# Performance work log

Hardware: AMD Instinct MI355X
Metric: run time of the kernel (lower is better)

The kernel has to match this reference:

```python
import jax, jax.numpy as jnp
import numpy as np

B, S, D, H, L = 16, 1024, 128, 8, 3
DFF = 4 * D  # 512
DH = D // H  # 16
NUM_CLASSES = 6


def layernorm(x, g, b, eps):
    mu = jnp.mean(x, axis=-1, keepdims=True)
    var = jnp.mean(jnp.square(x - mu), axis=-1, keepdims=True)
    return g * (x - mu) / jnp.sqrt(var + eps) + b


def setup_inputs() -> dict:
    key = jax.random.key(0)
    ks = jax.random.split(key, 16)
    sc = 0.05
    inp = {
        'x': jax.random.normal(ks[0], (B, S, D), dtype=jnp.float32),
        'Wq': jax.random.normal(ks[1], (L, D, D), dtype=jnp.float32) * sc,
        'bq': jnp.zeros((L, D), dtype=jnp.float32),
        'Wk': jax.random.normal(ks[2], (L, D, D), dtype=jnp.float32) * sc,
        'bk': jnp.zeros((L, D), dtype=jnp.float32),
        'Wv': jax.random.normal(ks[3], (L, D, D), dtype=jnp.float32) * sc,
        'bv': jnp.zeros((L, D), dtype=jnp.float32),
        'ln1_g': jnp.ones((L, D), dtype=jnp.float32),
        'ln1_b': jnp.zeros((L, D), dtype=jnp.float32),
        'W1': jax.random.normal(ks[4], (L, D, DFF), dtype=jnp.float32) * sc,
        'b1': jnp.zeros((L, DFF), dtype=jnp.float32),
        'W2': jax.random.normal(ks[5], (L, DFF, D), dtype=jnp.float32) * sc,
        'b2': jnp.zeros((L, D), dtype=jnp.float32),
        'ln2_g': jnp.ones((L, D), dtype=jnp.float32),
        'ln2_b': jnp.zeros((L, D), dtype=jnp.float32),
        'Wout': jax.random.normal(ks[6], (D, NUM_CLASSES), dtype=jnp.float32) * sc,
        'bout': jnp.zeros((NUM_CLASSES,), dtype=jnp.float32),
    }
    return inp


def reference(x, Wq, bq, Wk, bk, Wv, bv, ln1_g, ln1_b, W1, b1, W2, b2, ln2_g, ln2_b, Wout, bout):
    scale = 1.0 / jnp.sqrt(jnp.float32(DH))
    for l in range(L):
        # Q/K/V projections with ReLU activation (as in source Dense(..., relu))
        q = jax.nn.relu(jnp.einsum('bsd,de->bse', x, Wq[l]) + bq[l])
        k = jax.nn.relu(jnp.einsum('bsd,de->bse', x, Wk[l]) + bk[l])
        v = jax.nn.relu(jnp.einsum('bsd,de->bse', x, Wv[l]) + bv[l])
        # split-heads (tf.split axis=-1 / concat axis=0 == reshape to heads)
        qh = q.reshape(B, S, H, DH)
        kh = k.reshape(B, S, H, DH)
        vh = v.reshape(B, S, H, DH)
        scores = jnp.einsum('bqhd,bkhd->bhqk', qh, kh) * scale  # [B,H,S,S]
        attn = jax.nn.softmax(scores, axis=-1)
        o = jnp.einsum('bhqk,bkhd->bqhd', attn, vh).reshape(B, S, D)
        x = layernorm(o + x, ln1_g[l], ln1_b[l], 1e-8)
        # pointwise FFN (Conv1D kernel_size=1 == dense over last dim)
        h = jax.nn.relu(jnp.einsum('bsd,df->bsf', x, W1[l]) + b1[l])
        f = jnp.einsum('bsf,fd->bsd', h, W2[l]) + b2[l]
        x = layernorm(f + x, ln2_g[l], ln2_b[l], 1e-6)
    return jnp.einsum('bsd,dc->bsc', x, Wout) + bout
```

## Files before the change

### kernel.cpp

```cpp
#include <hip/hip_runtime.h>
#include <math.h>

#define Bq 16
#define Sq 1024
#define Dq 128
#define Hq 8
#define DHq 16
#define DFFq 512
#define Lq 3
#define NCLS 6
#define NROWS (Bq * Sq)
#define NX ((size_t)NROWS * Dq)

#define QSCL 0.36067376022224085f

typedef __attribute__((ext_vector_type(8))) short    bf16x8;
typedef __attribute__((ext_vector_type(4))) float    f32x4;
typedef __attribute__((ext_vector_type(4))) _Float16 f16x4;
typedef __attribute__((ext_vector_type(8))) _Float16 f16x8;

__device__ inline ushort f32_to_bf16(float f) {
    union { float f; unsigned u; } v; v.f = f;
    unsigned r = v.u + 0x7fffu + ((v.u >> 16) & 1u);
    return (ushort)(r >> 16);
}

__device__ __forceinline__ float exp2_raw(float x) {
    float r;
    asm("v_exp_f32 %0, %1" : "=v"(r) : "v"(x));
    return r;
}

__global__ __launch_bounds__(256) void prep_kernel(
    const float* __restrict__ Wqp, const float* __restrict__ Wkp,
    const float* __restrict__ Wvp, const float* __restrict__ W1p,
    const float* __restrict__ W2p, const float* __restrict__ xp,
    ushort* __restrict__ wbf, ushort* __restrict__ xbf)
{
    const int gid = blockIdx.x * 256 + threadIdx.x;
    if (gid < 147456) {
        const int w   = gid / 49152;
        const int rem = gid - w * 49152;
        const int l   = rem >> 14;
        const int idx = rem & 16383;
        const int k   = idx >> 7;
        const int n   = idx & 127;
        const float* src = (w == 0) ? Wqp : (w == 1) ? Wkp : Wvp;
        const float scl = (w == 0) ? QSCL : 1.0f;
        wbf[(size_t)(w * 3 + l) * 16384 + n * 128 + k] =
            f32_to_bf16(src[(size_t)l * 16384 + k * 128 + n] * scl);
    } else if (gid < 344064) {
        const int g   = gid - 147456;
        const int l   = g >> 16;
        const int idx = g & 65535;
        const int k   = idx >> 9;
        const int n   = idx & 511;
        wbf[147456 + (size_t)l * 65536 + n * 128 + k] =
            f32_to_bf16(W1p[(size_t)l * 65536 + k * 512 + n]);
    } else if (gid < 540672) {
        const int g   = gid - 344064;
        const int l   = g >> 16;
        const int idx = g & 65535;
        const int k   = idx >> 7;
        const int n   = idx & 127;
        wbf[344064 + (size_t)l * 65536 + n * 512 + k] =
            f32_to_bf16(W2p[(size_t)l * 65536 + k * 128 + n]);
    } else {
        const int g = gid - 540672;
        xbf[g] = f32_to_bf16(xp[g]);
    }
}

__global__ __launch_bounds__(256) void gemm_qkv(
    const ushort* __restrict__ A,
    const ushort* __restrict__ wq, const ushort* __restrict__ wk,
    const ushort* __restrict__ wv,
    const float* __restrict__ bqp, const float* __restrict__ bkp,
    const float* __restrict__ bvp,
    _Float16* __restrict__ qo, _Float16* __restrict__ ko,
    _Float16* __restrict__ vo)
{
    __shared__ ushort As[64 * 40];
    __shared__ ushort Bs[128 * 40];

    const int sel  = blockIdx.y;
    const ushort* Bt   = (sel == 0) ? wq : (sel == 1) ? wk : wv;
    const float*  bias = (sel == 0) ? bqp : (sel == 1) ? bkp : bvp;
    const float   bscl = (sel == 0) ? QSCL : 1.0f;

    const int tid  = threadIdx.x;
    const int row0 = blockIdx.x * 64;
    const int wave = tid >> 6;
    const int lane = tid & 63;
    const int quad = lane >> 4;
    const int m16  = lane & 15;
    const int wm   = wave >> 1;
    const int wn   = wave & 1;

    const int sar = tid >> 2;
    const int sac = (tid & 3) * 8;

    f32x4 acc[2][4];
    #pragma unroll
    for (int i = 0; i < 2; ++i)
        #pragma unroll
        for (int j = 0; j < 4; ++j) acc[i][j] = (f32x4)0.f;

    for (int k0 = 0; k0 < 128; k0 += 32) {
        bf16x8 av = *(const bf16x8*)(A + (size_t)(row0 + sar) * 128 + k0 + sac);
        const int r1 = tid >> 2, r2 = r1 + 64;
        bf16x8 bv1 = *(const bf16x8*)(Bt + (size_t)r1 * 128 + k0 + sac);
        bf16x8 bv2 = *(const bf16x8*)(Bt + (size_t)r2 * 128 + k0 + sac);

        __syncthreads();
        *(bf16x8*)&As[sar * 40 + sac] = av;
        *(bf16x8*)&Bs[r1 * 40 + sac]  = bv1;
        *(bf16x8*)&Bs[r2 * 40 + sac]  = bv2;
        __syncthreads();

        bf16x8 af[2], bf[4];
        #pragma unroll
        for (int i = 0; i < 2; ++i)
            af[i] = *(const bf16x8*)&As[(32 * wm + 16 * i + m16) * 40 + quad * 8];
        #pragma unroll
        for (int j = 0; j < 4; ++j)
            bf[j] = *(const bf16x8*)&Bs[(64 * wn + 16 * j + m16) * 40 + quad * 8];
        #pragma unroll
        for (int i = 0; i < 2; ++i)
            #pragma unroll
            for (int j = 0; j < 4; ++j)
                acc[i][j] = __builtin_amdgcn_mfma_f32_16x16x32_bf16(af[i], bf[j], acc[i][j], 0, 0, 0);
    }

    #pragma unroll
    for (int i = 0; i < 2; ++i) {
        #pragma unroll
        for (int j = 0; j < 4; ++j) {
            const int col = 64 * wn + 16 * j + m16;
            const float bb = bias[col] * bscl;
            const int hh = col >> 4, dh = col & 15;
            #pragma unroll
            for (int r = 0; r < 4; ++r) {
                float val = fmaxf(acc[i][j][r] + bb, 0.f);
                const int gr = row0 + 32 * wm + 16 * i + quad * 4 + r;
                const int b = gr >> 10, s = gr & 1023;
                if (sel == 2) {
                    vo[(((size_t)b * Hq + hh) * DHq + dh) * Sq + s] = (_Float16)val;
                } else {
                    _Float16* outp = (sel == 0) ? qo : ko;
                    outp[(((size_t)b * Hq + hh) * Sq + s) * DHq + dh] = (_Float16)val;
                }
            }
        }
    }
}

__global__ __launch_bounds__(256) void gemm_ffn_fused(
    const _Float16* __restrict__ o, const float* __restrict__ resid,
    const float* __restrict__ g1, const float* __restrict__ beta1,
    const ushort* __restrict__ W1t, const float* __restrict__ bias1,
    const ushort* __restrict__ W2t, const float* __restrict__ bias2,
    const float* __restrict__ g2, const float* __restrict__ beta2,
    float* __restrict__ xb,
    const ushort* __restrict__ wqn, const ushort* __restrict__ wkn,
    const ushort* __restrict__ wvn,
    const float* __restrict__ bqn, const float* __restrict__ bkn,
    const float* __restrict__ bvn,
    _Float16* __restrict__ qo, _Float16* __restrict__ ko,
    _Float16* __restrict__ vo, int do_next,
    const float* __restrict__ Wout, const float* __restrict__ bout,
    float* __restrict__ out, int last)
{
    __shared__ __align__(16) char smem[69120];
    ushort*    Af   = (ushort*)smem;
    ushort*    Hs   = (ushort*)(smem + 8704);
    ushort*    Bs   = (ushort*)(smem + 41984);
    float*     wo_s = (float*)(smem + 41984);
    _Float16*  vals = (_Float16*)(smem + 60416);
    float*     mus  = (float*)(smem + 68864);
    float*     rsds = (float*)(smem + 68992);

    const int tid  = threadIdx.x;
    const int row0 = blockIdx.x * 32;
    const int wave = tid >> 6;
    const int lane = tid & 63;
    const int quad = lane >> 4;
    const int m16  = lane & 15;
    const int wm   = wave >> 1;
    const int wn   = wave & 1;
    const int sac  = (tid & 3) * 8;
    const int r1   = tid >> 2, r2 = r1 + 64;

    #pragma unroll 2
    for (int it = 0; it < 8; ++it) {
        const int rr = wave * 8 + it;
        const size_t base = (size_t)(row0 + rr) * Dq;
        float v0 = (float)o[base + lane]      + resid[base + lane];
        float v1 = (float)o[base + 64 + lane] + resid[base + 64 + lane];

        float s = v0 + v1;
        #pragma unroll
        for (int off = 32; off > 0; off >>= 1) s += __shfl_xor(s, off, 64);
        const float mu = s * (1.f / 128.f);
        const float d0 = v0 - mu, d1 = v1 - mu;
        float vs = d0 * d0 + d1 * d1;
        #pragma unroll
        for (int off = 32; off > 0; off >>= 1) vs += __shfl_xor(vs, off, 64);
        const float rstd = rsqrtf(vs * (1.f / 128.f) + 1e-8f);

        const float rv0 = g1[lane]      * d0 * rstd + beta1[lane];
        const float rv1 = g1[lane + 64] * d1 * rstd + beta1[lane + 64];
        Af[rr * 136 + lane]        = f32_to_bf16(rv0);
        Af[rr * 136 + 64 + lane]   = f32_to_bf16(rv1);
        vals[rr * 132 + lane]      = (_Float16)rv0;
        vals[rr * 132 + 64 + lane] = (_Float16)rv1;
    }

    f32x4 acc[4];
    #pragma unroll
    for (int j = 0; j < 4; ++j) acc[j] = (f32x4)0.f;

    for (int idx = 0; idx < 8; ++idx) {
        const int cc = idx >> 1;
        const int k0 = (idx & 1) * 64;

        bf16x8 w11 = *(const bf16x8*)(W1t + (size_t)(cc * 128 + r1) * 128 + k0 + sac);
        bf16x8 w12 = *(const bf16x8*)(W1t + (size_t)(cc * 128 + r1) * 128 + k0 + 32 + sac);
        bf16x8 w21 = *(const bf16x8*)(W1t + (size_t)(cc * 128 + r2) * 128 + k0 + sac);
        bf16x8 w22 = *(const bf16x8*)(W1t + (size_t)(cc * 128 + r2) * 128 + k0 + 32 + sac);

        __syncthreads();
        *(bf16x8*)&Bs[r1 * 72 + sac]      = w11;
        *(bf16x8*)&Bs[r1 * 72 + 32 + sac] = w12;
        *(bf16x8*)&Bs[r2 * 72 + sac]      = w21;
        *(bf16x8*)&Bs[r2 * 72 + 32 + sac] = w22;
        __syncthreads();

        #pragma unroll
        for (int hh = 0; hh < 2; ++hh) {
            const int kk = k0 + hh * 32;
            const bf16x8 af = *(const bf16x8*)&Af[(16 * wm + m16) * 136 + kk + quad * 8];
            bf16x8 bf[4];
            #pragma unroll
            for (int j = 0; j < 4; ++j)
                bf[j] = *(const bf16x8*)&Bs[(64 * wn + 16 * j + m16) * 72 + hh * 32 + quad * 8];
            #pragma unroll
            for (int j = 0; j < 4; ++j)
                acc[j] = __builtin_amdgcn_mfma_f32_16x16x32_bf16(af, bf[j], acc[j], 0, 0, 0);
        }

        if (idx & 1) {
            #pragma unroll
            for (int j = 0; j < 4; ++j) {
                const int col = cc * 128 + 64 * wn + 16 * j + m16;
                const float bb = bias1[col];
                #pragma unroll
                for (int r = 0; r < 4; ++r) {
                    const int row = 16 * wm + quad * 4 + r;
                    Hs[row * 520 + col] = f32_to_bf16(fmaxf(acc[j][r] + bb, 0.f));
                }
                acc[j] = (f32x4)0.f;
            }
        }
    }

    f32x4 acc2[4];
    #pragma unroll
    for (int j = 0; j < 4; ++j) acc2[j] = (f32x4)0.f;

    for (int kc = 0; kc < 8; ++kc) {
        const int k0 = kc * 64;

        bf16x8 w11 = *(const bf16x8*)(W2t + (size_t)r1 * DFFq + k0 + sac);
        bf16x8 w12 = *(const bf16x8*)(W2t + (size_t)r1 * DFFq + k0 + 32 + sac);
        bf16x8 w21 = *(const bf16x8*)(W2t + (size_t)r2 * DFFq + k0 + sac);
        bf16x8 w22 = *(const bf16x8*)(W2t + (size_t)r2 * DFFq + k0 + 32 + sac);

        __syncthreads();
        *(bf16x8*)&Bs[r1 * 72 + sac]      = w11;
        *(bf16x8*)&Bs[r1 * 72 + 32 + sac] = w12;
        *(bf16x8*)&Bs[r2 * 72 + sac]      = w21;
        *(bf16x8*)&Bs[r2 * 72 + 32 + sac] = w22;
        __syncthreads();

        #pragma unroll
        for (int hh = 0; hh < 2; ++hh) {
            const int kk = k0 + hh * 32;
            const bf16x8 af = *(const bf16x8*)&Hs[(16 * wm + m16) * 520 + kk + quad * 8];
            bf16x8 bf[4];
            #pragma unroll
            for (int j = 0; j < 4; ++j)
                bf[j] = *(const bf16x8*)&Bs[(64 * wn + 16 * j + m16) * 72 + hh * 32 + quad * 8];
            #pragma unroll
            for (int j = 0; j < 4; ++j)
                acc2[j] = __builtin_amdgcn_mfma_f32_16x16x32_bf16(af, bf[j], acc2[j], 0, 0, 0);
        }
    }

    __syncthreads();

    float vreg[4][4];
    #pragma unroll
    for (int j = 0; j < 4; ++j) {
        const int col = 64 * wn + 16 * j + m16;
        const float bb = bias2[col];
        #pragma unroll
        for (int r = 0; r < 4; ++r) {
            const int row = 16 * wm + quad * 4 + r;
            float v = acc2[j][r] + bb + (float)vals[row * 132 + col];
            vreg[j][r] = v;
            vals[row * 132 + col] = (_Float16)v;
        }
    }
    if (last) {
        #pragma unroll
        for (int i = 0; i < 3; ++i) wo_s[tid + i * 256] = Wout[tid + i * 256];
    }
    __syncthreads();

    if (tid < 32) {
        float s = 0.f, s2 = 0.f;
        #pragma unroll 8
        for (int c = 0; c < Dq; ++c) {
            float x = (float)vals[tid * 132 + c];
            s += x; s2 = fmaf(x, x, s2);
        }
        const float mu  = s * (1.f / 128.f);
        const float var = s2 * (1.f / 128.f) - mu * mu;
        mus[tid]  = mu;
        rsds[tid] = rsqrtf(var + 1e-6f);
    }
    __syncthreads();

    if (!last) {
        #pragma unroll
        for (int j = 0; j < 4; ++j) {
            const int col = 64 * wn + 16 * j + m16;
            #pragma unroll
            for (int r = 0; r < 4; ++r) {
                const int row = 16 * wm + quad * 4 + r;
                const float rn = g2[col] * (vreg[j][r] - mus[row]) * rsds[row] + beta2[col];
                xb[(size_t)(row0 + row) * Dq + col] = rn;
                Af[row * 136 + col] = f32_to_bf16(rn);
            }
        }

        if (do_next) {
            for (int sel = 0; sel < 3; ++sel) {
                const ushort* Bt   = (sel == 0) ? wqn : (sel == 1) ? wkn : wvn;
                const float*  bias = (sel == 0) ? bqn : (sel == 1) ? bkn : bvn;
                const float   bscl = (sel == 0) ? QSCL : 1.0f;

                f32x4 qacc[4];
                #pragma unroll
                for (int j = 0; j < 4; ++j) qacc[j] = (f32x4)0.f;

                for (int half = 0; half < 2; ++half) {
                    const int k0 = half * 64;
                    bf16x8 w11 = *(const bf16x8*)(Bt + (size_t)r1 * 128 + k0 + sac);
                    bf16x8 w12 = *(const bf16x8*)(Bt + (size_t)r1 * 128 + k0 + 32 + sac);
                    bf16x8 w21 = *(const bf16x8*)(Bt + (size_t)r2 * 128 + k0 + sac);
                    bf16x8 w22 = *(const bf16x8*)(Bt + (size_t)r2 * 128 + k0 + 32 + sac);

                    __syncthreads();
                    *(bf16x8*)&Bs[r1 * 72 + sac]      = w11;
                    *(bf16x8*)&Bs[r1 * 72 + 32 + sac] = w12;
                    *(bf16x8*)&Bs[r2 * 72 + sac]      = w21;
                    *(bf16x8*)&Bs[r2 * 72 + 32 + sac] = w22;
                    __syncthreads();

                    #pragma unroll
                    for (int hh = 0; hh < 2; ++hh) {
                        const int kk = k0 + hh * 32;
                        const bf16x8 af = *(const bf16x8*)&Af[(16 * wm + m16) * 136 + kk + quad * 8];
                        bf16x8 bf[4];
                        #pragma unroll
                        for (int j = 0; j < 4; ++j)
                            bf[j] = *(const bf16x8*)&Bs[(64 * wn + 16 * j + m16) * 72 + hh * 32 + quad * 8];
                        #pragma unroll
                        for (int j = 0; j < 4; ++j)
                            qacc[j] = __builtin_amdgcn_mfma_f32_16x16x32_bf16(af, bf[j], qacc[j], 0, 0, 0);
                    }
                }

                #pragma unroll
                for (int j = 0; j < 4; ++j) {
                    const int col = 64 * wn + 16 * j + m16;
                    const float bb = bias[col] * bscl;
                    const int hh = col >> 4, dh = col & 15;
                    #pragma unroll
                    for (int r = 0; r < 4; ++r) {
                        float val = fmaxf(qacc[j][r] + bb, 0.f);
                        const int gr = row0 + 16 * wm + quad * 4 + r;
                        const int b = gr >> 10, s = gr & 1023;
                        if (sel == 2) {
                            vo[(((size_t)b * Hq + hh) * DHq + dh) * Sq + s] = (_Float16)val;
                        } else {
                            _Float16* outp = (sel == 0) ? qo : ko;
                            outp[(((size_t)b * Hq + hh) * Sq + s) * DHq + dh] = (_Float16)val;
                        }
                    }
                }
            }
        }
    } else {
        #pragma unroll
        for (int j = 0; j < 4; ++j) {
            const int col = 64 * wn + 16 * j + m16;
            #pragma unroll
            for (int r = 0; r < 4; ++r) {
                const int row = 16 * wm + quad * 4 + r;
                vals[row * 132 + col] =
                    (_Float16)(g2[col] * (vreg[j][r] - mus[row]) * rsds[row] + beta2[col]);
            }
        }
        __syncthreads();
        if (tid < 32 * NCLS) {
            const int row = tid / NCLS;
            const int c   = tid - row * NCLS;
            float a = bout[c];
            #pragma unroll 8
            for (int kk = 0; kk < Dq; ++kk)
                a = fmaf((float)vals[row * 132 + kk], wo_s[kk * NCLS + c], a);
            out[(size_t)(row0 + row) * NCLS + c] = a;
        }
    }
}

__global__ __launch_bounds__(256) void attn_mfma(
    const _Float16* __restrict__ q, const _Float16* __restrict__ k,
    const _Float16* __restrict__ vt, _Float16* __restrict__ o)
{
    __shared__ _Float16 Ks[256 * 20];
    __shared__ _Float16 Vs[16 * 264];

    const int bh   = blockIdx.x;
    const int qc   = blockIdx.y;
    const int b    = bh >> 3;
    const int h    = bh & 7;
    const int tid  = threadIdx.x;
    const int wave = tid >> 6;
    const int lane = tid & 63;
    const int quad = lane >> 4;
    const int m16  = lane & 15;
    const int q0   = qc * 128 + wave * 32;

    const f16x4 qf0 = *(const f16x4*)(q + (((size_t)bh * Sq) + q0 + m16) * DHq + quad * 4);
    const f16x4 qf1 = *(const f16x4*)(q + (((size_t)bh * Sq) + q0 + 16 + m16) * DHq + quad * 4);

    const _Float16* kg  = k  + (size_t)bh * Sq * DHq;
    const _Float16* vtg = vt + (size_t)bh * DHq * Sq;

    f32x4 oacc0 = (f32x4)0.f, oacc1 = (f32x4)0.f;
    float lacc0 = 0.f, lacc1 = 0.f;

    const int krow = tid;
    const int vrow = tid >> 4;
    const int vcol = (tid & 15) * 16;

    for (int kb = 0; kb < 4; ++kb) {
        f16x8 ka  = *(const f16x8*)(kg + ((size_t)kb * 256 + krow) * DHq);
        f16x8 kb8 = *(const f16x8*)(kg + ((size_t)kb * 256 + krow) * DHq + 8);
        f16x8 va  = *(const f16x8*)(vtg + (size_t)vrow * Sq + kb * 256 + vcol);
        f16x8 vb  = *(const f16x8*)(vtg + (size_t)vrow * Sq + kb * 256 + vcol + 8);
        __syncthreads();
        *(f16x8*)&Ks[krow * 20 + 0] = ka;
        *(f16x8*)&Ks[krow * 20 + 8] = kb8;
        *(f16x8*)&Vs[vrow * 264 + vcol + 0] = va;
        *(f16x8*)&Vs[vrow * 264 + vcol + 8] = vb;
        __syncthreads();

        #pragma unroll 4
        for (int kt = 0; kt < 16; ++kt) {
            const f16x4 kf = *(const f16x4*)&Ks[(kt * 16 + m16) * 20 + quad * 4];
            const f16x4 vf = *(const f16x4*)&Vs[m16 * 264 + kt * 16 + quad * 4];

            f32x4 st0 = __builtin_amdgcn_mfma_f32_16x16x16f16(kf, qf0, (f32x4)0.f, 0, 0, 0);
            f32x4 st1 = __builtin_amdgcn_mfma_f32_16x16x16f16(kf, qf1, (f32x4)0.f, 0, 0, 0);

            float p00 = exp2_raw(st0[0]);
            float p01 = exp2_raw(st0[1]);
            float p02 = exp2_raw(st0[2]);
            float p03 = exp2_raw(st0[3]);
            float p10 = exp2_raw(st1[0]);
            float p11 = exp2_raw(st1[1]);
            float p12 = exp2_raw(st1[2]);
            float p13 = exp2_raw(st1[3]);
            lacc0 += (p00 + p01) + (p02 + p03);
            lacc1 += (p10 + p11) + (p12 + p13);

            f16x4 pf0, pf1;
            pf0[0] = (_Float16)p00; pf0[1] = (_Float16)p01;
            pf0[2] = (_Float16)p02; pf0[3] = (_Float16)p03;
            pf1[0] = (_Float16)p10; pf1[1] = (_Float16)p11;
            pf1[2] = (_Float16)p12; pf1[3] = (_Float16)p13;

            oacc0 = __builtin_amdgcn_mfma_f32_16x16x16f16(pf0, vf, oacc0, 0, 0, 0);
            oacc1 = __builtin_amdgcn_mfma_f32_16x16x16f16(pf1, vf, oacc1, 0, 0, 0);
        }
    }

    lacc0 += __shfl_xor(lacc0, 16, 64);
    lacc0 += __shfl_xor(lacc0, 32, 64);
    lacc1 += __shfl_xor(lacc1, 16, 64);
    lacc1 += __shfl_xor(lacc1, 32, 64);

    #pragma unroll
    for (int r = 0; r < 4; ++r) {
        const float ls0 = __shfl(lacc0, quad * 4 + r, 64);
        const float ls1 = __shfl(lacc1, quad * 4 + r, 64);
        o[((size_t)b * Sq + q0 + quad * 4 + r) * Dq + h * DHq + m16]      = (_Float16)(oacc0[r] / ls0);
        o[((size_t)b * Sq + q0 + 16 + quad * 4 + r) * Dq + h * DHq + m16] = (_Float16)(oacc1[r] / ls1);
    }
}

extern "C" void kernel_launch(void* const* d_in, const int* in_sizes, int n_in,
                              void* d_out, int out_size, void* d_ws, size_t ws_size,
                              hipStream_t stream)
{
    const float* x_in  = (const float*)d_in[0];
    const float* Wq    = (const float*)d_in[1];
    const float* bq    = (const float*)d_in[2];
    const float* Wk    = (const float*)d_in[3];
    const float* bk    = (const float*)d_in[4];
    const float* Wv    = (const float*)d_in[5];
    const float* bv    = (const float*)d_in[6];
    const float* ln1_g = (const float*)d_in[7];
    const float* ln1_b = (const float*)d_in[8];
    const float* W1    = (const float*)d_in[9];
    const float* b1    = (const float*)d_in[10];
    const float* W2    = (const float*)d_in[11];
    const float* b2    = (const float*)d_in[12];
    const float* ln2_g = (const float*)d_in[13];
    const float* ln2_b = (const float*)d_in[14];
    const float* Wout  = (const float*)d_in[15];
    const float* bout  = (const float*)d_in[16];
    float* out = (float*)d_out;

    float* ws = (float*)d_ws;
    _Float16* qf16 = (_Float16*)ws;
    _Float16* kf16 = (_Float16*)(ws + NX / 2);
    _Float16* vt16 = (_Float16*)(ws + NX);
    float*    xb   = ws + 9 * NX / 2;
    ushort*   xbf0 = (ushort*)(ws + 11 * NX / 2);
    ushort*   wbf  = (ushort*)(ws + 7 * NX);
    _Float16* obuf = (_Float16*)(ws + 8 * NX);

    prep_kernel<<<dim3(10304), dim3(256), 0, stream>>>(Wq, Wk, Wv, W1, W2, x_in, wbf, xbf0);

    const dim3 blk(256);

    {
        const ushort* wqt = wbf + (size_t)0 * 16384;
        const ushort* wkt = wbf + (size_t)3 * 16384;
        const ushort* wvt = wbf + (size_t)6 * 16384;
        gemm_qkv<<<dim3(256, 3), blk, 0, stream>>>(
            xbf0, wqt, wkt, wvt, bq, bk, bv, qf16, kf16, vt16);
    }

    const float* xcur = x_in;
    for (int l = 0; l < Lq; ++l) {
        const ushort* w1t = wbf + 147456 + (size_t)l * 65536;
        const ushort* w2t = wbf + 344064 + (size_t)l * 65536;
        const int next = (l < Lq - 1) ? 1 : 0;
        const int ln   = l + 1;
        const ushort* wqn = next ? (wbf + (size_t)(0 * 3 + ln) * 16384) : wbf;
        const ushort* wkn = next ? (wbf + (size_t)(1 * 3 + ln) * 16384) : wbf;
        const ushort* wvn = next ? (wbf + (size_t)(2 * 3 + ln) * 16384) : wbf;
        const float*  bqn = next ? (bq + ln * Dq) : bq;
        const float*  bkn = next ? (bk + ln * Dq) : bk;
        const float*  bvn = next ? (bv + ln * Dq) : bv;

        attn_mfma<<<dim3(Bq * Hq, 8), blk, 0, stream>>>(qf16, kf16, vt16, obuf);

        gemm_ffn_fused<<<dim3(512), blk, 0, stream>>>(
            obuf, xcur, ln1_g + l * Dq, ln1_b + l * Dq,
            w1t, b1 + l * DFFq, w2t, b2 + l * Dq,
            ln2_g + l * Dq, ln2_b + l * Dq,
            xb,
            wqn, wkn, wvn, bqn, bkn, bvn,
            qf16, kf16, vt16, next,
            Wout, bout, out, (l == Lq - 1) ? 1 : 0);

        xcur = xb;
    }
}
```

Measured before the change: 254.8 us.

## Shrink FFN kernel shared memory by splitting hidden dim into halves

The fused LN+FFN kernel now processes the 512-wide hidden layer in two 256-column halves. It accumulates the second GEMM across halves, so the hidden buffer and the weight staging tile (now 32-wide K chunks) shrink and total LDS drops from about 69KB to about 36KB. Launch bounds request 4 blocks per CU. The residual is cached in registers and the LDS regions are aliased. This is meant to raise occupancy, at the cost of twice as many barrier-separated K steps with smaller loads each.

Measured after the change: 260.0 us. 2.0% more time.

```diff
diff --git a/kernel.cpp b/kernel.cpp
--- a/kernel.cpp
+++ b/kernel.cpp
@@ -155,7 +155,7 @@
     }
 }
 
-__global__ __launch_bounds__(256) void gemm_ffn_fused(
+__global__ __launch_bounds__(256, 4) void gemm_ffn_fused(
     const _Float16* __restrict__ o, const float* __restrict__ resid,
     const float* __restrict__ g1, const float* __restrict__ beta1,
     const ushort* __restrict__ W1t, const float* __restrict__ bias1,
@@ -171,14 +171,15 @@
     const float* __restrict__ Wout, const float* __restrict__ bout,
     float* __restrict__ out, int last)
 {
-    __shared__ __align__(16) char smem[69120];
-    ushort*    Af   = (ushort*)smem;
-    ushort*    Hs   = (ushort*)(smem + 8704);
-    ushort*    Bs   = (ushort*)(smem + 41984);
-    float*     wo_s = (float*)(smem + 41984);
-    _Float16*  vals = (_Float16*)(smem + 60416);
-    float*     mus  = (float*)(smem + 68864);
-    float*     rsds = (float*)(smem + 68992);
+    __shared__ __align__(16) char smem[36096];
+    ushort*    Af    = (ushort*)smem;
+    ushort*    Hs    = (ushort*)(smem + 8704);
+    ushort*    Bs    = (ushort*)(smem + 25600);
+    _Float16*  r16   = (_Float16*)(smem + 25600);
+    _Float16*  vals2 = (_Float16*)(smem + 8704);
+    float*     wo_s  = (float*)(smem + 25600);
+    float*     mus   = (float*)(smem + 35840);
+    float*     rsds  = (float*)(smem + 35968);
 
     const int tid  = threadIdx.x;
     const int row0 = blockIdx.x * 32;
@@ -210,87 +211,84 @@
 
         const float rv0 = g1[lane]      * d0 * rstd + beta1[lane];
         const float rv1 = g1[lane + 64] * d1 * rstd + beta1[lane + 64];
-        Af[rr * 136 + lane]        = f32_to_bf16(rv0);
-        Af[rr * 136 + 64 + lane]   = f32_to_bf16(rv1);
-        vals[rr * 132 + lane]      = (_Float16)rv0;
-        vals[rr * 132 + 64 + lane] = (_Float16)rv1;
-    }
-
-    f32x4 acc[4];
+        Af[rr * 136 + lane]       = f32_to_bf16(rv0);
+        Af[rr * 136 + 64 + lane]  = f32_to_bf16(rv1);
+        r16[rr * 132 + lane]      = (_Float16)rv0;
+        r16[rr * 132 + 64 + lane] = (_Float16)rv1;
+    }
+    __syncthreads();
+
+    float rreg[4][4];
     #pragma unroll
-    for (int j = 0; j < 4; ++j) acc[j] = (f32x4)0.f;
-
-    for (int idx = 0; idx < 8; ++idx) {
-        const int cc = idx >> 1;
-        const int k0 = (idx & 1) * 64;
-
-        bf16x8 w11 = *(const bf16x8*)(W1t + (size_t)(cc * 128 + r1) * 128 + k0 + sac);
-        bf16x8 w12 = *(const bf16x8*)(W1t + (size_t)(cc * 128 + r1) * 128 + k0 + 32 + sac);
-        bf16x8 w21 = *(const bf16x8*)(W1t + (size_t)(cc * 128 + r2) * 128 + k0 + sac);
-        bf16x8 w22 = *(const bf16x8*)(W1t + (size_t)(cc * 128 + r2) * 128 + k0 + 32 + sac);
-
-        __syncthreads();
-        *(bf16x8*)&Bs[r1 * 72 + sac]      = w11;
-        *(bf16x8*)&Bs[r1 * 72 + 32 + sac] = w12;
-        *(bf16x8*)&Bs[r2 * 72 + sac]      = w21;
-        *(bf16x8*)&Bs[r2 * 72 + 32 + sac] = w22;
-        __syncthreads();
-
-        #pragma unroll
-        for (int hh = 0; hh < 2; ++hh) {
-            const int kk = k0 + hh * 32;
-            const bf16x8 af = *(const bf16x8*)&Af[(16 * wm + m16) * 136 + kk + quad * 8];
-            bf16x8 bf[4];
-            #pragma unroll
-            for (int j = 0; j < 4; ++j)
-                bf[j] = *(const bf16x8*)&Bs[(64 * wn + 16 * j + m16) * 72 + hh * 32 + quad * 8];
-            #pragma unroll
-            for (int j = 0; j < 4; ++j)
-                acc[j] = __builtin_amdgcn_mfma_f32_16x16x32_bf16(af, bf[j], acc[j], 0, 0, 0);
-        }
-
-        if (idx & 1) {
-            #pragma unroll
-            for (int j = 0; j < 4; ++j) {
-                const int col = cc * 128 + 64 * wn + 16 * j + m16;
-                const float bb = bias1[col];
-                #pragma unroll
-                for (int r = 0; r < 4; ++r) {
-                    const int row = 16 * wm + quad * 4 + r;
-                    Hs[row * 520 + col] = f32_to_bf16(fmaxf(acc[j][r] + bb, 0.f));
-                }
-                acc[j] = (f32x4)0.f;
-            }
-        }
+    for (int j = 0; j < 4; ++j) {
+        const int col = 64 * wn + 16 * j + m16;
+        #pragma unroll
+        for (int r = 0; r < 4; ++r)
+            rreg[j][r] = (float)r16[(16 * wm + quad * 4 + r) * 132 + col];
     }
 
     f32x4 acc2[4];
     #pragma unroll
     for (int j = 0; j < 4; ++j) acc2[j] = (f32x4)0.f;
 
-    for (int kc = 0; kc < 8; ++kc) {
-        const int k0 = kc * 64;
-
-        bf16x8 w11 = *(const bf16x8*)(W2t + (size_t)r1 * DFFq + k0 + sac);
-        bf16x8 w12 = *(const bf16x8*)(W2t + (size_t)r1 * DFFq + k0 + 32 + sac);
-        bf16x8 w21 = *(const bf16x8*)(W2t + (size_t)r2 * DFFq + k0 + sac);
-        bf16x8 w22 = *(const bf16x8*)(W2t + (size_t)r2 * DFFq + k0 + 32 + sac);
-
-        __syncthreads();
-        *(bf16x8*)&Bs[r1 * 72 + sac]      = w11;
-        *(bf16x8*)&Bs[r1 * 72 + 32 + sac] = w12;
-        *(bf16x8*)&Bs[r2 * 72 + sac]      = w21;
-        *(bf16x8*)&Bs[r2 * 72 + 32 + sac] = w22;
-        __syncthreads();
-
-        #pragma unroll
-        for (int hh = 0; hh < 2; ++hh) {
-            const int kk = k0 + hh * 32;
-            const bf16x8 af = *(const bf16x8*)&Hs[(16 * wm + m16) * 520 + kk + quad * 8];
+    for (int half = 0; half < 2; ++half) {
+        f32x4 acc[4];
+        #pragma unroll
+        for (int j = 0; j < 4; ++j) acc[j] = (f32x4)0.f;
+
+        for (int idx = 0; idx < 8; ++idx) {
+            const int cc = idx >> 2;
+            const int k0 = (idx & 3) * 32;
+            const int gc0 = half * 256 + cc * 128;
+
+            bf16x8 wv1 = *(const bf16x8*)(W1t + (size_t)(gc0 + r1) * 128 + k0 + sac);
+            bf16x8 wv2 = *(const bf16x8*)(W1t + (size_t)(gc0 + r2) * 128 + k0 + sac);
+
+            __syncthreads();
+            *(bf16x8*)&Bs[r1 * 40 + sac] = wv1;
+            *(bf16x8*)&Bs[r2 * 40 + sac] = wv2;
+            __syncthreads();
+
+            const bf16x8 af = *(const bf16x8*)&Af[(16 * wm + m16) * 136 + k0 + quad * 8];
             bf16x8 bf[4];
             #pragma unroll
             for (int j = 0; j < 4; ++j)
-                bf[j] = *(const bf16x8*)&Bs[(64 * wn + 16 * j + m16) * 72 + hh * 32 + quad * 8];
+                bf[j] = *(const bf16x8*)&Bs[(64 * wn + 16 * j + m16) * 40 + quad * 8];
+            #pragma unroll
+            for (int j = 0; j < 4; ++j)
+                acc[j] = __builtin_amdgcn_mfma_f32_16x16x32_bf16(af, bf[j], acc[j], 0, 0, 0);
+
+            if ((idx & 3) == 3) {
+                #pragma unroll
+                for (int j = 0; j < 4; ++j) {
+                    const int lcol = cc * 128 + 64 * wn + 16 * j + m16;
+                    const float bb = bias1[half * 256 + lcol];
+                    #pragma unroll
+                    for (int r = 0; r < 4; ++r) {
+                        const int row = 16 * wm + quad * 4 + r;
+                        Hs[row * 264 + lcol] = f32_to_bf16(fmaxf(acc[j][r] + bb, 0.f));
+                    }
+                    acc[j] = (f32x4)0.f;
+                }
+            }
+        }
+
+        for (int kc = 0; kc < 8; ++kc) {
+            const int k0 = kc * 32;
+
+            bf16x8 wv1 = *(const bf16x8*)(W2t + (size_t)r1 * DFFq + half * 256 + k0 + sac);
+            bf16x8 wv2 = *(const bf16x8*)(W2t + (size_t)r2 * DFFq + half * 256 + k0 + sac);
+
+            __syncthreads();
+            *(bf16x8*)&Bs[r1 * 40 + sac] = wv1;
+            *(bf16x8*)&Bs[r2 * 40 + sac] = wv2;
+            __syncthreads();
+
+            const bf16x8 af = *(const bf16x8*)&Hs[(16 * wm + m16) * 264 + k0 + quad * 8];
+            bf16x8 bf[4];
+            #pragma unroll
+            for (int j = 0; j < 4; ++j)
+                bf[j] = *(const bf16x8*)&Bs[(64 * wn + 16 * j + m16) * 40 + quad * 8];
             #pragma unroll
             for (int j = 0; j < 4; ++j)
                 acc2[j] = __builtin_amdgcn_mfma_f32_16x16x32_bf16(af, bf[j], acc2[j], 0, 0, 0);
@@ -307,9 +305,9 @@
         #pragma unroll
         for (int r = 0; r < 4; ++r) {
             const int row = 16 * wm + quad * 4 + r;
-            float v = acc2[j][r] + bb + (float)vals[row * 132 + col];
+            float v = acc2[j][r] + bb + rreg[j][r];
             vreg[j][r] = v;
-            vals[row * 132 + col] = (_Float16)v;
+            vals2[row * 132 + col] = (_Float16)v;
         }
     }
     if (last) {
@@ -322,7 +320,7 @@
         float s = 0.f, s2 = 0.f;
         #pragma unroll 8
         for (int c = 0; c < Dq; ++c) {
-            float x = (float)vals[tid * 132 + c];
+            float x = (float)vals2[tid * 132 + c];
             s += x; s2 = fmaf(x, x, s2);
         }
         const float mu  = s * (1.f / 128.f);
@@ -355,32 +353,24 @@
                 #pragma unroll
                 for (int j = 0; j < 4; ++j) qacc[j] = (f32x4)0.f;
 
-                for (int half = 0; half < 2; ++half) {
-                    const int k0 = half * 64;
-                    bf16x8 w11 = *(const bf16x8*)(Bt + (size_t)r1 * 128 + k0 + sac);
-                    bf16x8 w12 = *(const bf16x8*)(Bt + (size_t)r1 * 128 + k0 + 32 + sac);
-                    bf16x8 w21 = *(const bf16x8*)(Bt + (size_t)r2 * 128 + k0 + sac);
-                    bf16x8 w22 = *(const bf16x8*)(Bt + (size_t)r2 * 128 + k0 + 32 + sac);
+                for (int kc = 0; kc < 4; ++kc) {
+                    const int k0 = kc * 32;
+                    bf16x8 wv1 = *(const bf16x8*)(Bt + (size_t)r1 * 128 + k0 + sac);
+                    bf16x8 wv2 = *(const bf16x8*)(Bt + (size_t)r2 * 128 + k0 + sac);
 
                     __syncthreads();
-                    *(bf16x8*)&Bs[r1 * 72 + sac]      = w11;
-                    *(bf16x8*)&Bs[r1 * 72 + 32 + sac] = w12;
-                    *(bf16x8*)&Bs[r2 * 72 + sac]      = w21;
-                    *(bf16x8*)&Bs[r2 * 72 + 32 + sac] = w22;
+                    *(bf16x8*)&Bs[r1 * 40 + sac] = wv1;
+                    *(bf16x8*)&Bs[r2 * 40 + sac] = wv2;
                     __syncthreads();
 
+                    const bf16x8 af = *(const bf16x8*)&Af[(16 * wm + m16) * 136 + k0 + quad * 8];
+                    bf16x8 bf[4];
                     #pragma unroll
-                    for (int hh = 0; hh < 2; ++hh) {
-                        const int kk = k0 + hh * 32;
-                        const bf16x8 af = *(const bf16x8*)&Af[(16 * wm + m16) * 136 + kk + quad * 8];
-                        bf16x8 bf[4];
-                        #pragma unroll
-                        for (int j = 0; j < 4; ++j)
-                            bf[j] = *(const bf16x8*)&Bs[(64 * wn + 16 * j + m16) * 72 + hh * 32 + quad * 8];
-                        #pragma unroll
-                        for (int j = 0; j < 4; ++j)
-                            qacc[j] = __builtin_amdgcn_mfma_f32_16x16x32_bf16(af, bf[j], qacc[j], 0, 0, 0);
-                    }
+                    for (int j = 0; j < 4; ++j)
+                        bf[j] = *(const bf16x8*)&Bs[(64 * wn + 16 * j + m16) * 40 + quad * 8];
+                    #pragma unroll
+                    for (int j = 0; j < 4; ++j)
+                        qacc[j] = __builtin_amdgcn_mfma_f32_16x16x32_bf16(af, bf[j], qacc[j], 0, 0, 0);
                 }
 
                 #pragma unroll
@@ -410,7 +400,7 @@
             #pragma unroll
             for (int r = 0; r < 4; ++r) {
                 const int row = 16 * wm + quad * 4 + r;
-                vals[row * 132 + col] =
+                vals2[row * 132 + col] =
                     (_Float16)(g2[col] * (vreg[j][r] - mus[row]) * rsds[row] + beta2[col]);
             }
         }
@@ -421,7 +411,7 @@
             float a = bout[c];
             #pragma unroll 8
             for (int kk = 0; kk < Dq; ++kk)
-                a = fmaf((float)vals[row * 132 + kk], wo_s[kk * NCLS + c], a);
+                a = fmaf((float)vals2[row * 132 + kk], wo_s[kk * NCLS + c], a);
             out[(size_t)(row0 + row) * NCLS + c] = a;
         }
     }
```

## Split FFN hidden dimension in halves to shrink LDS and raise occupancy

Applied to the files above, without the earlier changes.

The fused FFN kernel now processes the 512-wide hidden layer in two 256-column halves. Each half computes its slice of H and immediately accumulates it into the second GEMM, so the H buffer in shared memory is halved. The residual is moved into registers and several LDS regions are aliased, cutting shared memory from about 69KB to about 44KB, and launch bounds request 3 blocks per CU. The intent is higher occupancy to hide latency, at the cost of extra register pressure from the min-blocks hint and an added barrier.

After: 256.4 us. About the same (+0.6%).

```diff
diff --git a/kernel.cpp b/kernel.cpp
--- a/kernel.cpp
+++ b/kernel.cpp
@@ -155,7 +155,7 @@
     }
 }
 
-__global__ __launch_bounds__(256) void gemm_ffn_fused(
+__global__ __launch_bounds__(256, 3) void gemm_ffn_fused(
     const _Float16* __restrict__ o, const float* __restrict__ resid,
     const float* __restrict__ g1, const float* __restrict__ beta1,
     const ushort* __restrict__ W1t, const float* __restrict__ bias1,
@@ -171,14 +171,15 @@
     const float* __restrict__ Wout, const float* __restrict__ bout,
     float* __restrict__ out, int last)
 {
-    __shared__ __align__(16) char smem[69120];
-    ushort*    Af   = (ushort*)smem;
-    ushort*    Hs   = (ushort*)(smem + 8704);
-    ushort*    Bs   = (ushort*)(smem + 41984);
-    float*     wo_s = (float*)(smem + 41984);
-    _Float16*  vals = (_Float16*)(smem + 60416);
-    float*     mus  = (float*)(smem + 68864);
-    float*     rsds = (float*)(smem + 68992);
+    __shared__ __align__(16) char smem[44288];
+    ushort*    Af    = (ushort*)smem;
+    ushort*    Hs    = (ushort*)(smem + 8704);
+    ushort*    Bs    = (ushort*)(smem + 25600);
+    _Float16*  r16   = (_Float16*)(smem + 25600);
+    _Float16*  vals2 = (_Float16*)(smem + 8704);
+    float*     wo_s  = (float*)(smem + 25600);
+    float*     mus   = (float*)(smem + 44032);
+    float*     rsds  = (float*)(smem + 44160);
 
     const int tid  = threadIdx.x;
     const int row0 = blockIdx.x * 32;
@@ -210,90 +211,103 @@
 
         const float rv0 = g1[lane]      * d0 * rstd + beta1[lane];
         const float rv1 = g1[lane + 64] * d1 * rstd + beta1[lane + 64];
-        Af[rr * 136 + lane]        = f32_to_bf16(rv0);
-        Af[rr * 136 + 64 + lane]   = f32_to_bf16(rv1);
-        vals[rr * 132 + lane]      = (_Float16)rv0;
-        vals[rr * 132 + 64 + lane] = (_Float16)rv1;
-    }
-
-    f32x4 acc[4];
+        Af[rr * 136 + lane]       = f32_to_bf16(rv0);
+        Af[rr * 136 + 64 + lane]  = f32_to_bf16(rv1);
+        r16[rr * 132 + lane]      = (_Float16)rv0;
+        r16[rr * 132 + 64 + lane] = (_Float16)rv1;
+    }
+    __syncthreads();
+
+    float rreg[4][4];
     #pragma unroll
-    for (int j = 0; j < 4; ++j) acc[j] = (f32x4)0.f;
-
-    for (int idx = 0; idx < 8; ++idx) {
-        const int cc = idx >> 1;
-        const int k0 = (idx & 1) * 64;
-
-        bf16x8 w11 = *(const bf16x8*)(W1t + (size_t)(cc * 128 + r1) * 128 + k0 + sac);
-        bf16x8 w12 = *(const bf16x8*)(W1t + (size_t)(cc * 128 + r1) * 128 + k0 + 32 + sac);
-        bf16x8 w21 = *(const bf16x8*)(W1t + (size_t)(cc * 128 + r2) * 128 + k0 + sac);
-        bf16x8 w22 = *(const bf16x8*)(W1t + (size_t)(cc * 128 + r2) * 128 + k0 + 32 + sac);
-
-        __syncthreads();
-        *(bf16x8*)&Bs[r1 * 72 + sac]      = w11;
-        *(bf16x8*)&Bs[r1 * 72 + 32 + sac] = w12;
-        *(bf16x8*)&Bs[r2 * 72 + sac]      = w21;
-        *(bf16x8*)&Bs[r2 * 72 + 32 + sac] = w22;
-        __syncthreads();
-
-        #pragma unroll
-        for (int hh = 0; hh < 2; ++hh) {
-            const int kk = k0 + hh * 32;
-            const bf16x8 af = *(const bf16x8*)&Af[(16 * wm + m16) * 136 + kk + quad * 8];
-            bf16x8 bf[4];
-            #pragma unroll
-            for (int j = 0; j < 4; ++j)
-                bf[j] = *(const bf16x8*)&Bs[(64 * wn + 16 * j + m16) * 72 + hh * 32 + quad * 8];
-            #pragma unroll
-            for (int j = 0; j < 4; ++j)
-                acc[j] = __builtin_amdgcn_mfma_f32_16x16x32_bf16(af, bf[j], acc[j], 0, 0, 0);
-        }
-
-        if (idx & 1) {
-            #pragma unroll
-            for (int j = 0; j < 4; ++j) {
-                const int col = cc * 128 + 64 * wn + 16 * j + m16;
-                const float bb = bias1[col];
-                #pragma unroll
-                for (int r = 0; r < 4; ++r) {
-                    const int row = 16 * wm + quad * 4 + r;
-                    Hs[row * 520 + col] = f32_to_bf16(fmaxf(acc[j][r] + bb, 0.f));
-                }
-                acc[j] = (f32x4)0.f;
-            }
-        }
+    for (int j = 0; j < 4; ++j) {
+        const int col = 64 * wn + 16 * j + m16;
+        #pragma unroll
+        for (int r = 0; r < 4; ++r)
+            rreg[j][r] = (float)r16[(16 * wm + quad * 4 + r) * 132 + col];
     }
 
     f32x4 acc2[4];
     #pragma unroll
     for (int j = 0; j < 4; ++j) acc2[j] = (f32x4)0.f;
 
-    for (int kc = 0; kc < 8; ++kc) {
-        const int k0 = kc * 64;
-
-        bf16x8 w11 = *(const bf16x8*)(W2t + (size_t)r1 * DFFq + k0 + sac);
-        bf16x8 w12 = *(const bf16x8*)(W2t + (size_t)r1 * DFFq + k0 + 32 + sac);
-        bf16x8 w21 = *(const bf16x8*)(W2t + (size_t)r2 * DFFq + k0 + sac);
-        bf16x8 w22 = *(const bf16x8*)(W2t + (size_t)r2 * DFFq + k0 + 32 + sac);
-
-        __syncthreads();
-        *(bf16x8*)&Bs[r1 * 72 + sac]      = w11;
-        *(bf16x8*)&Bs[r1 * 72 + 32 + sac] = w12;
-        *(bf16x8*)&Bs[r2 * 72 + sac]      = w21;
-        *(bf16x8*)&Bs[r2 * 72 + 32 + sac] = w22;
-        __syncthreads();
-
-        #pragma unroll
-        for (int hh = 0; hh < 2; ++hh) {
-            const int kk = k0 + hh * 32;
-            const bf16x8 af = *(const bf16x8*)&Hs[(16 * wm + m16) * 520 + kk + quad * 8];
-            bf16x8 bf[4];
+    for (int half = 0; half < 2; ++half) {
+        f32x4 acc[4];
+        #pragma unroll
+        for (int j = 0; j < 4; ++j) acc[j] = (f32x4)0.f;
+
+        for (int idx = 0; idx < 4; ++idx) {
+            const int cc = idx >> 1;
+            const int k0 = (idx & 1) * 64;
+            const int gc0 = half * 256 + cc * 128;
+
+            bf16x8 w11 = *(const bf16x8*)(W1t + (size_t)(gc0 + r1) * 128 + k0 + sac);
+            bf16x8 w12 = *(const bf16x8*)(W1t + (size_t)(gc0 + r1) * 128 + k0 + 32 + sac);
+            bf16x8 w21 = *(const bf16x8*)(W1t + (size_t)(gc0 + r2) * 128 + k0 + sac);
+            bf16x8 w22 = *(const bf16x8*)(W1t + (size_t)(gc0 + r2) * 128 + k0 + 32 + sac);
+
+            __syncthreads();
+            *(bf16x8*)&Bs[r1 * 72 + sac]      = w11;
+            *(bf16x8*)&Bs[r1 * 72 + 32 + sac] = w12;
+            *(bf16x8*)&Bs[r2 * 72 + sac]      = w21;
+            *(bf16x8*)&Bs[r2 * 72 + 32 + sac] = w22;
+            __syncthreads();
+
             #pragma unroll
-            for (int j = 0; j < 4; ++j)
-                bf[j] = *(const bf16x8*)&Bs[(64 * wn + 16 * j + m16) * 72 + hh * 32 + quad * 8];
+            for (int hh = 0; hh < 2; ++hh) {
+                const int kk = k0 + hh * 32;
+                const bf16x8 af = *(const bf16x8*)&Af[(16 * wm + m16) * 136 + kk + quad * 8];
+                bf16x8 bf[4];
+                #pragma unroll
+                for (int j = 0; j < 4; ++j)
+                    bf[j] = *(const bf16x8*)&Bs[(64 * wn + 16 * j + m16) * 72 + hh * 32 + quad * 8];
+                #pragma unroll
+                for (int j = 0; j < 4; ++j)
+                    acc[j] = __builtin_amdgcn_mfma_f32_16x16x32_bf16(af, bf[j], acc[j], 0, 0, 0);
+            }
+
+            if (idx & 1) {
+                #pragma unroll
+                for (int j = 0; j < 4; ++j) {
+                    const int lcol = cc * 128 + 64 * wn + 16 * j + m16;
+                    const float bb = bias1[half * 256 + lcol];
+                    #pragma unroll
+                    for (int r = 0; r < 4; ++r) {
+                        const int row = 16 * wm + quad * 4 + r;
+                        Hs[row * 264 + lcol] = f32_to_bf16(fmaxf(acc[j][r] + bb, 0.f));
+                    }
+                    acc[j] = (f32x4)0.f;
+                }
+            }
+        }
+
+        for (int kc = 0; kc < 4; ++kc) {
+            const int k0 = kc * 64;
+
+            bf16x8 w11 = *(const bf16x8*)(W2t + (size_t)r1 * DFFq + half * 256 + k0 + sac);
+            bf16x8 w12 = *(const bf16x8*)(W2t + (size_t)r1 * DFFq + half * 256 + k0 + 32 + sac);
+            bf16x8 w21 = *(const bf16x8*)(W2t + (size_t)r2 * DFFq + half * 256 + k0 + sac);
+            bf16x8 w22 = *(const bf16x8*)(W2t + (size_t)r2 * DFFq + half * 256 + k0 + 32 + sac);
+
+            __syncthreads();
+            *(bf16x8*)&Bs[r1 * 72 + sac]      = w11;
+            *(bf16x8*)&Bs[r1 * 72 + 32 + sac] = w12;
+            *(bf16x8*)&Bs[r2 * 72 + sac]      = w21;
+            *(bf16x8*)&Bs[r2 * 72 + 32 + sac] = w22;
+            __syncthreads();
+
             #pragma unroll
-            for (int j = 0; j < 4; ++j)
-                acc2[j] = __builtin_amdgcn_mfma_f32_16x16x32_bf16(af, bf[j], acc2[j], 0, 0, 0);
+            for (int hh = 0; hh < 2; ++hh) {
+                const int kk = k0 + hh * 32;
+                const bf16x8 af = *(const bf16x8*)&Hs[(16 * wm + m16) * 264 + kk + quad * 8];
+                bf16x8 bf[4];
+                #pragma unroll
+                for (int j = 0; j < 4; ++j)
+                    bf[j] = *(const bf16x8*)&Bs[(64 * wn + 16 * j + m16) * 72 + hh * 32 + quad * 8];
+                #pragma unroll
+                for (int j = 0; j < 4; ++j)
+                    acc2[j] = __builtin_amdgcn_mfma_f32_16x16x32_bf16(af, bf[j], acc2[j], 0, 0, 0);
+            }
         }
     }
 
@@ -307,9 +321,9 @@
         #pragma unroll
         for (int r = 0; r < 4; ++r) {
             const int row = 16 * wm + quad * 4 + r;
-            float v = acc2[j][r] + bb + (float)vals[row * 132 + col];
+            float v = acc2[j][r] + bb + rreg[j][r];
             vreg[j][r] = v;
-            vals[row * 132 + col] = (_Float16)v;
+            vals2[row * 132 + col] = (_Float16)v;
         }
     }
     if (last) {
@@ -322,7 +336,7 @@
         float s = 0.f, s2 = 0.f;
         #pragma unroll 8
         for (int c = 0; c < Dq; ++c) {
-            float x = (float)vals[tid * 132 + c];
+            float x = (float)vals2[tid * 132 + c];
             s += x; s2 = fmaf(x, x, s2);
         }
         const float mu  = s * (1.f / 128.f);
@@ -355,8 +369,8 @@
                 #pragma unroll
                 for (int j = 0; j < 4; ++j) qacc[j] = (f32x4)0.f;
 
-                for (int half = 0; half < 2; ++half) {
-                    const int k0 = half * 64;
+                for (int kc = 0; kc < 2; ++kc) {
+                    const int k0 = kc * 64;
                     bf16x8 w11 = *(const bf16x8*)(Bt + (size_t)r1 * 128 + k0 + sac);
                     bf16x8 w12 = *(const bf16x8*)(Bt + (size_t)r1 * 128 + k0 + 32 + sac);
                     bf16x8 w21 = *(const bf16x8*)(Bt + (size_t)r2 * 128 + k0 + sac);
@@ -410,7 +424,7 @@
             #pragma unroll
             for (int r = 0; r < 4; ++r) {
                 const int row = 16 * wm + quad * 4 + r;
-                vals[row * 132 + col] =
+                vals2[row * 132 + col] =
                     (_Float16)(g2[col] * (vreg[j][r] - mus[row]) * rsds[row] + beta2[col]);
             }
         }
@@ -421,7 +435,7 @@
             float a = bout[c];
             #pragma unroll 8
             for (int kk = 0; kk < Dq; ++kk)
-                a = fmaf((float)vals[row * 132 + kk], wo_s[kk * NCLS + c], a);
+                a = fmaf((float)vals2[row * 132 + kk], wo_s[kk * NCLS + c], a);
             out[(size_t)(row0 + row) * NCLS + c] = a;
         }
     }
```
